# Kernel tuning notes

Hardware: AMD Instinct MI355X
Metric: run time of the kernel (lower is better)

## Reference

```python
import jax, jax.numpy as jnp
import numpy as np

ALPHA = 0.2  # LeakyReLU negative slope
NEG_BIG = -9e15


def setup_inputs() -> dict:
    key = jax.random.key(0)
    k_h, k_adj, k_W, k_a = jax.random.split(key, 4)
    B, N, F_in, F_out = 8, 2048, 128, 64
    h = jax.random.normal(k_h, (B, N, F_in), dtype=jnp.float32)
    adj = jax.random.randint(k_adj, (B, N, N), 0, 2, dtype=jnp.int32)
    # xavier_uniform: bound = sqrt(6/(fan_in+fan_out))
    bW = float(np.sqrt(6.0 / (F_in + F_out)))
    W = jax.random.uniform(k_W, (F_in, F_out), dtype=jnp.float32, minval=-bW, maxval=bW)
    ba = float(np.sqrt(6.0 / (2 * F_out + 1)))
    a = jax.random.uniform(k_a, (2 * F_out, 1), dtype=jnp.float32, minval=-ba, maxval=ba)
    return {"h": h, "adj": adj, "W": W, "a": a}


def reference(h, adj, W, a):
    # h: [B,N,Fin], adj: [B,N,N], W: [Fin,Fout], a: [2*Fout,1]
    F_out = W.shape[1]
    Wh = jnp.einsum('bnf,fo->bno', h, W)               # [B,N,Fout]
    a1 = a[:F_out, 0]                                   # [Fout] (source/i part)
    a2 = a[F_out:, 0]                                   # [Fout] (target/j part)
    # e_ij = leakyrelu(Wh_i . a1 + Wh_j . a2) -- avoids O(N^2*2F) concat
    si = Wh @ a1                                        # [B,N]
    sj = Wh @ a2                                        # [B,N]
    e = si[:, :, None] + sj[:, None, :]                 # [B,N,N]
    e = jnp.where(e > 0, e, ALPHA * e)                  # LeakyReLU
    e = jnp.where(adj > 0, e, NEG_BIG)                  # mask non-edges
    attention = jax.nn.softmax(e, axis=2)               # [B,N,N]
    # dropout omitted (eval / training=False)
    h_prime = jnp.einsum('bij,bjo->bio', attention, Wh)  # [B,N,Fout]
    return h_prime
```

## Files before the change

kernel.cpp:

```cpp
#include <hip/hip_runtime.h>
#include <hip/hip_bf16.h>

#define ALPHA 0.2f
#define LOG2E 1.4426950408889634f

typedef __attribute__((ext_vector_type(8))) short bf16x8;
typedef __attribute__((ext_vector_type(4))) float f32x4;
typedef __attribute__((ext_vector_type(4))) int i32x4;

__device__ __forceinline__ int cvt_pk_bf16(float lo, float hi) {
    int r;
    asm("v_cvt_pk_bf16_f32 %0, %1, %2" : "=v"(r) : "v"(lo), "v"(hi));
    return r;
}

__device__ __forceinline__ void stage16(const void* g, void* l) {
    __builtin_amdgcn_global_load_lds(
        (const __attribute__((address_space(1))) void*)g,
        (__attribute__((address_space(3))) void*)l, 16, 0, 0);
}

__global__ __launch_bounds__(256) void gat_precompute(
    const float* __restrict__ h, const float* __restrict__ W,
    const float* __restrict__ a, unsigned short* __restrict__ WhF,
    float* __restrict__ si2, float* __restrict__ sj2)
{
    __shared__ float h_lds[32][128];
    __shared__ float wh_lds[32][65];
    const int tid  = threadIdx.x;
    const int lane = tid & 63;
    const int wave = tid >> 6;
    const long long row0 = (long long)blockIdx.x * 32;

    {
        const float4* s4 = (const float4*)(h + row0 * 128);
        #pragma unroll
        for (int i = 0; i < 4; ++i) {
            int idx = tid + i * 256;
            float4 v = s4[idx];
            *(float4*)&h_lds[idx >> 5][(idx & 31) * 4] = v;
        }
    }
    __syncthreads();

    const float a1 = a[lane];
    const float a2 = a[64 + lane];
    float acc[8];
    #pragma unroll
    for (int r = 0; r < 8; ++r) acc[r] = 0.0f;

    for (int f = 0; f < 128; f += 4) {
        const float w0 = W[(f+0)*64 + lane];
        const float w1 = W[(f+1)*64 + lane];
        const float w2 = W[(f+2)*64 + lane];
        const float w3 = W[(f+3)*64 + lane];
        #pragma unroll
        for (int r = 0; r < 8; ++r) {
            const float4 hv = *(const float4*)&h_lds[wave*8 + r][f];
            acc[r] = fmaf(hv.x, w0, acc[r]);
            acc[r] = fmaf(hv.y, w1, acc[r]);
            acc[r] = fmaf(hv.z, w2, acc[r]);
            acc[r] = fmaf(hv.w, w3, acc[r]);
        }
    }

    #pragma unroll
    for (int r = 0; r < 8; ++r) {
        const int rr = wave*8 + r;
        wh_lds[rr][lane] = acc[r];
        float s1 = acc[r] * a1;
        float s2 = acc[r] * a2;
        #pragma unroll
        for (int off = 32; off > 0; off >>= 1) {
            s1 += __shfl_xor(s1, off);
            s2 += __shfl_xor(s2, off);
        }
        if (lane == 0) {
            si2[row0 + rr] = s1 * LOG2E;
            sj2[row0 + rr] = s2 * LOG2E;
        }
    }
    __syncthreads();

    const long long b  = row0 >> 11;
    const int jcb  = (int)((row0 & 2047) >> 5);
    const int ob   = tid >> 6;
    const int ln   = tid & 63;
    const int ar   = ln & 15;
    const int gg   = ln >> 4;
    i32x4 pk;
    #pragma unroll
    for (int k = 0; k < 4; ++k)
        pk[k] = cvt_pk_bf16(wh_lds[gg*8 + 2*k    ][ob*16 + ar],
                            wh_lds[gg*8 + 2*k + 1][ob*16 + ar]);
    *(i32x4*)(WhF + ((b*64 + jcb)*4 + ob)*512 + ln*8) = pk;
}

__global__ __launch_bounds__(256, 4) void gat_attention(
    const int* __restrict__ adj, const unsigned short* __restrict__ WhF,
    const float* __restrict__ si2, const float* __restrict__ sj2,
    float* __restrict__ out)
{
    __shared__ char ldsbuf[16640];
    const int tid  = threadIdx.x;
    const int lane = tid & 63;
    const int wave = tid >> 6;
    const int b    = blockIdx.x & 7;
    const int i0   = (int)((blockIdx.x >> 3) << 4);
    const int arow = lane & 15;
    const int g    = lane >> 4;
    const long long bN = (long long)b * 2048;

    const int* asrc0;
    const int* asrc1;
    {
        int r = lane >> 3;
        int u = (lane & 7) ^ (r & 7);
        asrc0 = adj + (bN + i0 + r)*2048 + wave*512 + u*4;
        int r2 = 8 + (lane >> 3);
        int u2 = (lane & 7) ^ (r2 & 7);
        asrc1 = adj + (bN + i0 + r2)*2048 + wave*512 + u2*4;
    }

    const unsigned short* fbase =
        WhF + ((long long)(b*64 + wave*16) * 4) * 512 + lane*8;

    const float* sjb = sj2 + bN;
    float mx = -INFINITY;
    #pragma unroll 4
    for (int i = 0; i < 32; ++i) mx = fmaxf(mx, sjb[lane + i*64]);
    #pragma unroll
    for (int off = 32; off > 0; off >>= 1) mx = fmaxf(mx, __shfl_xor(mx, off));

    const float si_r = si2[bN + i0 + arow];
    const float u0f  = si_r + mx;
    const float m2   = fmaxf(u0f, ALPHA * u0f);
    const float Ci   = si_r - m2;
    const float Di   = ALPHA * si_r - m2;

    const float* sjq = sjb + wave*512 + g*8;

    f32x4 accf[4];
    #pragma unroll
    for (int ob = 0; ob < 4; ++ob) accf[ob] = (f32x4){0.f,0.f,0.f,0.f};
    f32x4 accl = (f32x4){0.f,0.f,0.f,0.f};
    bf16x8 ones;
    #pragma unroll
    for (int k = 0; k < 8; ++k) ones[k] = (short)0x3F80;

    bf16x8 cb0, cb1, cb2, cb3, nb0, nb1, nb2, nb3;

    #define STAGE(S, STEP) { \
        char* base_ = ldsbuf + (S)*8192 + wave*2048; \
        stage16(asrc0 + (STEP)*32, base_); \
        stage16(asrc1 + (STEP)*32, base_ + 1024); \
    }

    #define LOADB(D0, D1, D2, D3, STEP) { \
        D0 = *(const bf16x8*)(fbase + ((STEP)*4 + 0)*512); \
        D1 = *(const bf16x8*)(fbase + ((STEP)*4 + 1)*512); \
        D2 = *(const bf16x8*)(fbase + ((STEP)*4 + 2)*512); \
        D3 = *(const bf16x8*)(fbase + ((STEP)*4 + 3)*512); \
    }

    #define BODY(S, STEP) { \
        const char* ab = ldsbuf + (S)*8192 + wave*2048; \
        const i32x4 A0 = *(const i32x4*)(ab + arow*128 + ((g*2    ) ^ (arow & 7))*16); \
        const i32x4 A1 = *(const i32x4*)(ab + arow*128 + ((g*2 + 1) ^ (arow & 7))*16); \
        const f32x4 S0 = *(const f32x4*)(sjq + (STEP)*32); \
        const f32x4 S1 = *(const f32x4*)(sjq + (STEP)*32 + 4); \
        float p[8]; \
        _Pragma("unroll") \
        for (int e = 0; e < 4; ++e) { \
            float pe = __builtin_amdgcn_exp2f( \
                fmaxf(Ci + S0[e], fmaf(ALPHA, S0[e], Di))); \
            p[e] = (A0[e] > 0) ? pe : 0.0f; \
        } \
        _Pragma("unroll") \
        for (int e = 0; e < 4; ++e) { \
            float pe = __builtin_amdgcn_exp2f( \
                fmaxf(Ci + S1[e], fmaf(ALPHA, S1[e], Di))); \
            p[4+e] = (A1[e] > 0) ? pe : 0.0f; \
        } \
        i32x4 pk_; \
        pk_[0] = cvt_pk_bf16(p[0], p[1]); \
        pk_[1] = cvt_pk_bf16(p[2], p[3]); \
        pk_[2] = cvt_pk_bf16(p[4], p[5]); \
        pk_[3] = cvt_pk_bf16(p[6], p[7]); \
        const bf16x8 pa = __builtin_bit_cast(bf16x8, pk_); \
        accl    = __builtin_amdgcn_mfma_f32_16x16x32_bf16(pa, ones, accl,    0, 0, 0); \
        accf[0] = __builtin_amdgcn_mfma_f32_16x16x32_bf16(pa, cb0, accf[0], 0, 0, 0); \
        accf[1] = __builtin_amdgcn_mfma_f32_16x16x32_bf16(pa, cb1, accf[1], 0, 0, 0); \
        accf[2] = __builtin_amdgcn_mfma_f32_16x16x32_bf16(pa, cb2, accf[2], 0, 0, 0); \
        accf[3] = __builtin_amdgcn_mfma_f32_16x16x32_bf16(pa, cb3, accf[3], 0, 0, 0); \
    }

    STAGE(0, 0);
    LOADB(cb0, cb1, cb2, cb3, 0);
    __syncthreads();

    int s = 0;
    for (int st = 0; st < 15; ++st) {
        STAGE(s^1, st+1);
        LOADB(nb0, nb1, nb2, nb3, st+1);
        BODY(s, st);
        __syncthreads();
        cb0 = nb0; cb1 = nb1; cb2 = nb2; cb3 = nb3;
        s ^= 1;
    }
    BODY(s, 15);

    __syncthreads();
    float* accb = (float*)ldsbuf;
    float* lb   = (float*)(ldsbuf + 16384);
    #pragma unroll
    for (int ob = 0; ob < 4; ++ob)
        #pragma unroll
        for (int reg = 0; reg < 4; ++reg)
            accb[(wave*16 + g*4 + reg)*64 + ob*16 + arow] = accf[ob][reg];
    if (arow == 0) {
        #pragma unroll
        for (int reg = 0; reg < 4; ++reg)
            lb[wave*16 + g*4 + reg] = accl[reg];
    }
    __syncthreads();

    const int r  = tid >> 4;
    const int c0 = (tid & 15) * 4;
    const float L = lb[r] + lb[16 + r] + lb[32 + r] + lb[48 + r];
    const float inv = 1.0f / L;
    float4 v;
    v.x = (accb[r*64 + c0 + 0] + accb[(16+r)*64 + c0 + 0]
         + accb[(32+r)*64 + c0 + 0] + accb[(48+r)*64 + c0 + 0]) * inv;
    v.y = (accb[r*64 + c0 + 1] + accb[(16+r)*64 + c0 + 1]
         + accb[(32+r)*64 + c0 + 1] + accb[(48+r)*64 + c0 + 1]) * inv;
    v.z = (accb[r*64 + c0 + 2] + accb[(16+r)*64 + c0 + 2]
         + accb[(32+r)*64 + c0 + 2] + accb[(48+r)*64 + c0 + 2]) * inv;
    v.w = (accb[r*64 + c0 + 3] + accb[(16+r)*64 + c0 + 3]
         + accb[(32+r)*64 + c0 + 3] + accb[(48+r)*64 + c0 + 3]) * inv;
    *(float4*)(out + (bN + i0 + r)*64 + c0) = v;
}

extern "C" void kernel_launch(void* const* d_in, const int* in_sizes, int n_in,
                              void* d_out, int out_size, void* d_ws, size_t ws_size,
                              hipStream_t stream) {
    const float* h   = (const float*)d_in[0];
    const int*   adj = (const int*)d_in[1];
    const float* W   = (const float*)d_in[2];
    const float* a   = (const float*)d_in[3];
    float* out = (float*)d_out;

    unsigned short* WhF = (unsigned short*)d_ws;
    float* si2 = (float*)((char*)d_ws + (size_t)16384*64*2);
    float* sj2 = si2 + 16384;

    gat_precompute<<<512, 256, 0, stream>>>(h, W, a, WhF, si2, sj2);
    gat_attention<<<1024, 256, 0, stream>>>(adj, WhF, si2, sj2, out);
}
```

Baseline: 45.22 us.

## Load adjacency directly into registers with 3-deep prefetch instead of LDS staging

Replaces the global_load_lds staging of adjacency tiles and the per-step block barriers with direct per-lane vector loads into a 3-slot register ring. The loop is fully unrolled and sj values are prefetched alongside. This removes LDS traffic and the __syncthreads in the main loop, at the cost of more registers; the launch-bounds occupancy hint is dropped. Each lane now reads 32 contiguous bytes per row, so global coalescing differs from the swizzled staged pattern.

```diff
diff --git a/kernel.cpp b/kernel.cpp
--- a/kernel.cpp
+++ b/kernel.cpp
@@ -12,12 +12,6 @@
     int r;
     asm("v_cvt_pk_bf16_f32 %0, %1, %2" : "=v"(r) : "v"(lo), "v"(hi));
     return r;
-}
-
-__device__ __forceinline__ void stage16(const void* g, void* l) {
-    __builtin_amdgcn_global_load_lds(
-        (const __attribute__((address_space(1))) void*)g,
-        (__attribute__((address_space(3))) void*)l, 16, 0, 0);
 }
 
 __global__ __launch_bounds__(256) void gat_precompute(
@@ -96,7 +90,7 @@
     *(i32x4*)(WhF + ((b*64 + jcb)*4 + ob)*512 + ln*8) = pk;
 }
 
-__global__ __launch_bounds__(256, 4) void gat_attention(
+__global__ __launch_bounds__(256) void gat_attention(
     const int* __restrict__ adj, const unsigned short* __restrict__ WhF,
     const float* __restrict__ si2, const float* __restrict__ sj2,
     float* __restrict__ out)
@@ -111,17 +105,8 @@
     const int g    = lane >> 4;
     const long long bN = (long long)b * 2048;
 
-    const int* asrc0;
-    const int* asrc1;
-    {
-        int r = lane >> 3;
-        int u = (lane & 7) ^ (r & 7);
-        asrc0 = adj + (bN + i0 + r)*2048 + wave*512 + u*4;
-        int r2 = 8 + (lane >> 3);
-        int u2 = (lane & 7) ^ (r2 & 7);
-        asrc1 = adj + (bN + i0 + r2)*2048 + wave*512 + u2*4;
-    }
-
+    const int*   aptr = adj + (bN + i0 + arow)*2048 + wave*512 + g*8;
+    const float* sjq  = sj2 + bN + wave*512 + g*8;
     const unsigned short* fbase =
         WhF + ((long long)(b*64 + wave*16) * 4) * 512 + lane*8;
 
@@ -138,8 +123,6 @@
     const float Ci   = si_r - m2;
     const float Di   = ALPHA * si_r - m2;
 
-    const float* sjq = sjb + wave*512 + g*8;
-
     f32x4 accf[4];
     #pragma unroll
     for (int ob = 0; ob < 4; ++ob) accf[ob] = (f32x4){0.f,0.f,0.f,0.f};
@@ -148,14 +131,16 @@
     #pragma unroll
     for (int k = 0; k < 8; ++k) ones[k] = (short)0x3F80;
 
+    i32x4 A0[3], A1[3];
+    f32x4 S0[3], S1[3];
     bf16x8 cb0, cb1, cb2, cb3, nb0, nb1, nb2, nb3;
 
-    #define STAGE(S, STEP) { \
-        char* base_ = ldsbuf + (S)*8192 + wave*2048; \
-        stage16(asrc0 + (STEP)*32, base_); \
-        stage16(asrc1 + (STEP)*32, base_ + 1024); \
-    }
-
+    #define LOADA(SLOT, STEP) { \
+        A0[SLOT] = *(const i32x4*)(aptr + (STEP)*32); \
+        A1[SLOT] = *(const i32x4*)(aptr + (STEP)*32 + 4); \
+        S0[SLOT] = *(const f32x4*)(sjq + (STEP)*32); \
+        S1[SLOT] = *(const f32x4*)(sjq + (STEP)*32 + 4); \
+    }
     #define LOADB(D0, D1, D2, D3, STEP) { \
         D0 = *(const bf16x8*)(fbase + ((STEP)*4 + 0)*512); \
         D1 = *(const bf16x8*)(fbase + ((STEP)*4 + 1)*512); \
@@ -163,54 +148,49 @@
         D3 = *(const bf16x8*)(fbase + ((STEP)*4 + 3)*512); \
     }
 
-    #define BODY(S, STEP) { \
-        const char* ab = ldsbuf + (S)*8192 + wave*2048; \
-        const i32x4 A0 = *(const i32x4*)(ab + arow*128 + ((g*2    ) ^ (arow & 7))*16); \
-        const i32x4 A1 = *(const i32x4*)(ab + arow*128 + ((g*2 + 1) ^ (arow & 7))*16); \
-        const f32x4 S0 = *(const f32x4*)(sjq + (STEP)*32); \
-        const f32x4 S1 = *(const f32x4*)(sjq + (STEP)*32 + 4); \
-        float p[8]; \
-        _Pragma("unroll") \
-        for (int e = 0; e < 4; ++e) { \
-            float pe = __builtin_amdgcn_exp2f( \
-                fmaxf(Ci + S0[e], fmaf(ALPHA, S0[e], Di))); \
-            p[e] = (A0[e] > 0) ? pe : 0.0f; \
-        } \
-        _Pragma("unroll") \
-        for (int e = 0; e < 4; ++e) { \
-            float pe = __builtin_amdgcn_exp2f( \
-                fmaxf(Ci + S1[e], fmaf(ALPHA, S1[e], Di))); \
-            p[4+e] = (A1[e] > 0) ? pe : 0.0f; \
-        } \
-        i32x4 pk_; \
-        pk_[0] = cvt_pk_bf16(p[0], p[1]); \
-        pk_[1] = cvt_pk_bf16(p[2], p[3]); \
-        pk_[2] = cvt_pk_bf16(p[4], p[5]); \
-        pk_[3] = cvt_pk_bf16(p[6], p[7]); \
-        const bf16x8 pa = __builtin_bit_cast(bf16x8, pk_); \
-        accl    = __builtin_amdgcn_mfma_f32_16x16x32_bf16(pa, ones, accl,    0, 0, 0); \
-        accf[0] = __builtin_amdgcn_mfma_f32_16x16x32_bf16(pa, cb0, accf[0], 0, 0, 0); \
-        accf[1] = __builtin_amdgcn_mfma_f32_16x16x32_bf16(pa, cb1, accf[1], 0, 0, 0); \
-        accf[2] = __builtin_amdgcn_mfma_f32_16x16x32_bf16(pa, cb2, accf[2], 0, 0, 0); \
-        accf[3] = __builtin_amdgcn_mfma_f32_16x16x32_bf16(pa, cb3, accf[3], 0, 0, 0); \
-    }
-
-    STAGE(0, 0);
+    LOADA(0, 0);
+    LOADA(1, 1);
     LOADB(cb0, cb1, cb2, cb3, 0);
-    __syncthreads();
-
-    int s = 0;
-    for (int st = 0; st < 15; ++st) {
-        STAGE(s^1, st+1);
-        LOADB(nb0, nb1, nb2, nb3, st+1);
-        BODY(s, st);
-        __syncthreads();
+
+    #pragma unroll
+    for (int st = 0; st < 16; ++st) {
+        if (st < 14) LOADA((st + 2) % 3, st + 2);
+        if (st < 15) LOADB(nb0, nb1, nb2, nb3, st + 1);
+
+        const i32x4 cA0 = A0[st % 3];
+        const i32x4 cA1 = A1[st % 3];
+        const f32x4 cS0 = S0[st % 3];
+        const f32x4 cS1 = S1[st % 3];
+
+        float p[8];
+        #pragma unroll
+        for (int e = 0; e < 4; ++e) {
+            float pe = __builtin_amdgcn_exp2f(
+                fmaxf(Ci + cS0[e], fmaf(ALPHA, cS0[e], Di)));
+            p[e] = (cA0[e] > 0) ? pe : 0.0f;
+        }
+        #pragma unroll
+        for (int e = 0; e < 4; ++e) {
+            float pe = __builtin_amdgcn_exp2f(
+                fmaxf(Ci + cS1[e], fmaf(ALPHA, cS1[e], Di)));
+            p[4+e] = (cA1[e] > 0) ? pe : 0.0f;
+        }
+        i32x4 pk_;
+        pk_[0] = cvt_pk_bf16(p[0], p[1]);
+        pk_[1] = cvt_pk_bf16(p[2], p[3]);
+        pk_[2] = cvt_pk_bf16(p[4], p[5]);
+        pk_[3] = cvt_pk_bf16(p[6], p[7]);
+        const bf16x8 pa = __builtin_bit_cast(bf16x8, pk_);
+
+        accl    = __builtin_amdgcn_mfma_f32_16x16x32_bf16(pa, ones, accl,    0, 0, 0);
+        accf[0] = __builtin_amdgcn_mfma_f32_16x16x32_bf16(pa, cb0, accf[0], 0, 0, 0);
+        accf[1] = __builtin_amdgcn_mfma_f32_16x16x32_bf16(pa, cb1, accf[1], 0, 0, 0);
+        accf[2] = __builtin_amdgcn_mfma_f32_16x16x32_bf16(pa, cb2, accf[2], 0, 0, 0);
+        accf[3] = __builtin_amdgcn_mfma_f32_16x16x32_bf16(pa, cb3, accf[3], 0, 0, 0);
+
         cb0 = nb0; cb1 = nb1; cb2 = nb2; cb3 = nb3;
-        s ^= 1;
-    }
-    BODY(s, 15);
-
-    __syncthreads();
+    }
+
     float* accb = (float*)ldsbuf;
     float* lb   = (float*)(ldsbuf + 16384);
     #pragma unroll
```

After: 51.09 us. 1.13x slower.
